# Kernel tuning notes

Measured on AMD Instinct MI355X. Metric: run time of the kernel, lower is better.

## Reference

```python
import jax, jax.numpy as jnp
import numpy as np

B, T, I = 32768, 28, 28
H, C = 128, 10


def setup_inputs() -> dict:
    key = jax.random.key(0)
    ks = jax.random.split(key, 7)
    s_u = 1.0 / np.sqrt(I)
    s_w = 1.0 / np.sqrt(H)
    return {
        "x": jax.random.normal(ks[0], (B, T, I), dtype=jnp.float32),
        "U_w": jax.random.uniform(ks[1], (H, I), jnp.float32, -s_u, s_u),
        "U_b": jax.random.uniform(ks[2], (H,), jnp.float32, -s_u, s_u),
        "W_w": jax.random.uniform(ks[3], (H, H), jnp.float32, -s_w, s_w),
        "W_b": jax.random.uniform(ks[4], (H,), jnp.float32, -s_w, s_w),
        "V_w": jax.random.uniform(ks[5], (C, H), jnp.float32, -s_w, s_w),
        "V_b": jax.random.uniform(ks[6], (C,), jnp.float32, -s_w, s_w),
    }


def reference(x, U_w, U_b, W_w, W_b, V_w, V_b):
    # x: [B, T, I]. Precompute input projections for all timesteps at once
    # (one big GEMM), then scan the sequential recurrence on S.
    ux = jnp.einsum("bti,hi->tbh", x, U_w) + U_b  # [T, B, H]

    def step(S, ux_t):
        S = jnp.tanh(ux_t + S @ W_w.T + W_b)
        return S, None

    S0 = jnp.zeros((x.shape[0], W_w.shape[0]), dtype=x.dtype)
    S_final, _ = jax.lax.scan(step, S0, ux)
    return S_final @ V_w.T + V_b  # [B, C]
```

## Files before the change

kernel.cpp:

```cpp
#include <hip/hip_runtime.h>


#define T_STEPS 28
#define S_STRIDE 132

typedef __attribute__((ext_vector_type(4))) float f32x4;
typedef __attribute__((ext_vector_type(8))) short short8;

#define MFMA16 __builtin_amdgcn_mfma_f32_16x16x32_bf16

__device__ __forceinline__ unsigned pack2(float lo, float hi) {
#if __has_builtin(__builtin_amdgcn_cvt_pk_bf16_f32)
  auto p = __builtin_amdgcn_cvt_pk_bf16_f32(lo, hi);
  return __builtin_bit_cast(unsigned, p);
#else
  unsigned a = __builtin_bit_cast(unsigned, lo);
  a += 0x7FFFu + ((a >> 16) & 1u);
  unsigned b = __builtin_bit_cast(unsigned, hi);
  b += 0x7FFFu + ((b >> 16) & 1u);
  return (a >> 16) | (b & 0xFFFF0000u);
#endif
}

__device__ __forceinline__ short8 to_frag(f32x4 a, f32x4 b) {
  union { unsigned u[4]; short8 v; } r;
  r.u[0] = pack2(a[0], a[1]);
  r.u[1] = pack2(a[2], a[3]);
  r.u[2] = pack2(b[0], b[1]);
  r.u[3] = pack2(b[2], b[3]);
  return r.v;
}

__device__ __forceinline__ short8 load_frag64(const unsigned short* sp, int off) {
  union { uint2 d[2]; short8 v; } r;
  r.d[0] = *(const uint2*)(sp + off);
  r.d[1] = *(const uint2*)(sp + off + 4);
  return r.v;
}

__device__ __forceinline__ f32x4 tanh4(f32x4 z) {
  f32x4 x2 = z * z;
  f32x4 p = 945.0f + x2 * (105.0f + x2);
  f32x4 q = 945.0f + x2 * (420.0f + 15.0f * x2);
  f32x4 num = z * p;
  f32x4 r;
#pragma unroll
  for (int i = 0; i < 4; ++i) r[i] = __builtin_amdgcn_rcpf(q[i]);
  f32x4 t = num * r;
#pragma unroll
  for (int i = 0; i < 4; ++i) t[i] = __builtin_amdgcn_fmed3f(t[i], -1.0f, 1.0f);
  return t;
}

__global__ __launch_bounds__(256, 4) void rnn_fused(
    const float* __restrict__ x,  const float* __restrict__ Uw,
    const float* __restrict__ Ub, const float* __restrict__ Ww,
    const float* __restrict__ Wb, const float* __restrict__ Vw,
    const float* __restrict__ Vb, float* __restrict__ out) {
  __shared__ __align__(16) unsigned short Sbuf[2][16 * S_STRIDE];

  const int tid  = threadIdx.x;
  const int w    = tid >> 6;
  const int lane = tid & 63;
  const int l15  = lane & 15;
  const int q    = lane >> 4;
  const int mrow = w * 32;
  const int b0   = blockIdx.x * 16;

  const f32x4 zero4 = {0.f, 0.f, 0.f, 0.f};

  const float* xp = x + (size_t)(b0 + l15) * 784 + q * 8;
  f32x4 xa = *(const f32x4*)xp;
  f32x4 xb = zero4;
  if (q < 3) xb = *(const f32x4*)(xp + 4);

  short8 wfrag[2][4];
  short8 ufrag[2];
  f32x4  bias[2];
#pragma unroll
  for (int mt = 0; mt < 2; ++mt) {
    const int h = mrow + mt * 16 + l15;
    const float* wp = Ww + h * 128 + q * 8;
#pragma unroll
    for (int kt = 0; kt < 4; ++kt) {
      wfrag[mt][kt] = to_frag(*(const f32x4*)wp, *(const f32x4*)(wp + 4));
      wp += 32;
    }
    const float* up = Uw + h * 28 + q * 8;
    f32x4 u0 = *(const f32x4*)up;
    f32x4 u1 = zero4;
    if (q < 3) u1 = *(const f32x4*)(up + 4);
    ufrag[mt] = to_frag(u0, u1);
    const int hb = mrow + mt * 16 + q * 4;
    bias[mt] = *(const f32x4*)(Wb + hb) + *(const f32x4*)(Ub + hb);
  }

  const int ro = l15 * S_STRIDE;

  {
    short8 xf = to_frag(xa, xb);
    const float* x1 = xp + 28;
    xa = *(const f32x4*)x1;
    if (q < 3) xb = *(const f32x4*)(x1 + 4);
    unsigned short* wp = &Sbuf[1][0];
#pragma unroll
    for (int mt = 0; mt < 2; ++mt) {
      f32x4 d0 = MFMA16(ufrag[mt], xf, bias[mt], 0, 0, 0);
      f32x4 t0 = tanh4(d0);
      uint2 dd; dd.x = pack2(t0[0], t0[1]); dd.y = pack2(t0[2], t0[3]);
      *(uint2*)(wp + ro + mrow + mt * 16 + q * 4) = dd;
    }
  }
  __syncthreads();

  const float* xn = xp + 56;
  f32x4 acc[2];
#pragma unroll 1
  for (int t = 1; t < T_STEPS; ++t) {
    short8 xf = to_frag(xa, xb);
    if (t < T_STEPS - 1) {
      xa = *(const f32x4*)xn;
      if (q < 3) xb = *(const f32x4*)(xn + 4);
      xn += 28;
    }

    const unsigned short* sp = &Sbuf[t & 1][0] + ro + q * 8;

    short8 sA = load_frag64(sp, 0);
#pragma unroll
    for (int mt = 0; mt < 2; ++mt)
      acc[mt] = MFMA16(wfrag[mt][0], sA, bias[mt], 0, 0, 0);
#pragma unroll
    for (int kt = 1; kt < 4; ++kt) {
      sA = load_frag64(sp, kt * 32);
#pragma unroll
      for (int mt = 0; mt < 2; ++mt)
        acc[mt] = MFMA16(wfrag[mt][kt], sA, acc[mt], 0, 0, 0);
    }
#pragma unroll
    for (int mt = 0; mt < 2; ++mt)
      acc[mt] = MFMA16(ufrag[mt], xf, acc[mt], 0, 0, 0);

    unsigned short* wp = &Sbuf[(t + 1) & 1][0];
#pragma unroll
    for (int mt = 0; mt < 2; ++mt) {
      f32x4 th = tanh4(acc[mt]);
      uint2 dd; dd.x = pack2(th[0], th[1]); dd.y = pack2(th[2], th[3]);
      *(uint2*)(wp + ro + mrow + mt * 16 + q * 4) = dd;
    }
    __syncthreads();
  }

  {
    const int r  = tid >> 4;
    const int c0 = tid & 15;
    if (c0 < 10) {
      const float* vp = Vw + c0 * 128;
      const unsigned short* srow = &Sbuf[0][0] + r * S_STRIDE;
      float a0 = Vb[c0];
#pragma unroll
      for (int h = 0; h < 128; h += 4) {
        uint2 d  = *(const uint2*)(srow + h);
        f32x4 v4 = *(const f32x4*)(vp + h);
        a0 += __builtin_bit_cast(float, d.x << 16) * v4[0];
        a0 += __builtin_bit_cast(float, d.x & 0xFFFF0000u) * v4[1];
        a0 += __builtin_bit_cast(float, d.y << 16) * v4[2];
        a0 += __builtin_bit_cast(float, d.y & 0xFFFF0000u) * v4[3];
      }
      out[(size_t)(b0 + r) * 10 + c0] = a0;
    }
  }
}

extern "C" void kernel_launch(void* const* d_in, const int* in_sizes, int n_in,
                              void* d_out, int out_size, void* d_ws, size_t ws_size,
                              hipStream_t stream) {
  const float* x  = (const float*)d_in[0];
  const float* Uw = (const float*)d_in[1];
  const float* Ub = (const float*)d_in[2];
  const float* Ww = (const float*)d_in[3];
  const float* Wb = (const float*)d_in[4];
  const float* Vw = (const float*)d_in[5];
  const float* Vb = (const float*)d_in[6];
  rnn_fused<<<2048, 256, 0, stream>>>(x, Uw, Ub, Ww, Wb, Vw, Vb, (float*)d_out);
}
```

Measured before the change: 216.0 us.

## Stage x timesteps into LDS in cooperative bf16 chunks

Replaces the per-timestep global loads of x, each wave loading its own fragment, with block-cooperative staging of 10-timestep chunks into a shared bf16 buffer. The block's 16 rows are read as contiguous float4 slots and converted once, and each step then reads its input fragment from LDS. The aim is better-coalesced global reads and less redundant conversion and load latency on the serial recurrence. The cost is extra LDS, which may reduce occupancy, plus two extra syncs where each chunk's global loads now sit on the critical path instead of being prefetched a step ahead.

Result: no change. 218.8 us (+1.3%).

```diff
diff --git a/kernel.cpp b/kernel.cpp
--- a/kernel.cpp
+++ b/kernel.cpp
@@ -3,6 +3,7 @@
 
 #define T_STEPS 28
 #define S_STRIDE 132
+#define X_STRIDE 324
 
 typedef __attribute__((ext_vector_type(4))) float f32x4;
 typedef __attribute__((ext_vector_type(8))) short short8;
@@ -52,12 +53,45 @@
   return t;
 }
 
+template <int NT>
+__device__ __forceinline__ void stage_chunk(const float* __restrict__ xblk,
+                                            unsigned short* __restrict__ Xb,
+                                            int tid, int t0) {
+  constexpr int SLOTS = 16 * NT * 7;
+  constexpr int ITERS = (SLOTS + 255) / 256;
+  f32x4 xr[ITERS];
+#pragma unroll
+  for (int k = 0; k < ITERS; ++k) {
+    const int s = tid + 256 * k;
+    if (s < SLOTS) {
+      const int row = s / (NT * 7), g = s - row * (NT * 7);
+      const int tt = g / 7, j = g - tt * 7;
+      xr[k] = *(const f32x4*)(xblk + row * 784 + (t0 + tt) * 28 + j * 4);
+    }
+  }
+#pragma unroll
+  for (int k = 0; k < ITERS; ++k) {
+    const int s = tid + 256 * k;
+    if (s < SLOTS) {
+      const int row = s / (NT * 7), g = s - row * (NT * 7);
+      const int tt = g / 7, j = g - tt * 7;
+      uint2 d; d.x = pack2(xr[k][0], xr[k][1]); d.y = pack2(xr[k][2], xr[k][3]);
+      *(uint2*)(Xb + row * X_STRIDE + tt * 32 + j * 4) = d;
+      if (j == 0) {
+        uint2 zz; zz.x = 0u; zz.y = 0u;
+        *(uint2*)(Xb + row * X_STRIDE + tt * 32 + 28) = zz;
+      }
+    }
+  }
+}
+
 __global__ __launch_bounds__(256, 4) void rnn_fused(
     const float* __restrict__ x,  const float* __restrict__ Uw,
     const float* __restrict__ Ub, const float* __restrict__ Ww,
     const float* __restrict__ Wb, const float* __restrict__ Vw,
     const float* __restrict__ Vb, float* __restrict__ out) {
   __shared__ __align__(16) unsigned short Sbuf[2][16 * S_STRIDE];
+  __shared__ __align__(16) unsigned short Xbuf[16 * X_STRIDE];
 
   const int tid  = threadIdx.x;
   const int w    = tid >> 6;
@@ -68,11 +102,9 @@
   const int b0   = blockIdx.x * 16;
 
   const f32x4 zero4 = {0.f, 0.f, 0.f, 0.f};
-
-  const float* xp = x + (size_t)(b0 + l15) * 784 + q * 8;
-  f32x4 xa = *(const f32x4*)xp;
-  f32x4 xb = zero4;
-  if (q < 3) xb = *(const f32x4*)(xp + 4);
+  const float* xblk = x + (size_t)b0 * 784;
+
+  stage_chunk<10>(xblk, Xbuf, tid, 0);
 
   short8 wfrag[2][4];
   short8 ufrag[2];
@@ -94,14 +126,43 @@
     const int hb = mrow + mt * 16 + q * 4;
     bias[mt] = *(const f32x4*)(Wb + hb) + *(const f32x4*)(Ub + hb);
   }
+  __syncthreads();
 
   const int ro = l15 * S_STRIDE;
+  const int xo = l15 * X_STRIDE + q * 8;
+  f32x4 acc[2];
+
+  auto step = [&](int t, int tt) {
+    short8 xf = load_frag64(&Xbuf[0], xo + tt * 32);
+    const unsigned short* sp = &Sbuf[t & 1][0] + ro + q * 8;
+
+    short8 sA = load_frag64(sp, 0);
+#pragma unroll
+    for (int mt = 0; mt < 2; ++mt)
+      acc[mt] = MFMA16(wfrag[mt][0], sA, bias[mt], 0, 0, 0);
+#pragma unroll
+    for (int kt = 1; kt < 4; ++kt) {
+      sA = load_frag64(sp, kt * 32);
+#pragma unroll
+      for (int mt = 0; mt < 2; ++mt)
+        acc[mt] = MFMA16(wfrag[mt][kt], sA, acc[mt], 0, 0, 0);
+    }
+#pragma unroll
+    for (int mt = 0; mt < 2; ++mt)
+      acc[mt] = MFMA16(ufrag[mt], xf, acc[mt], 0, 0, 0);
+
+    unsigned short* wp = &Sbuf[(t + 1) & 1][0];
+#pragma unroll
+    for (int mt = 0; mt < 2; ++mt) {
+      f32x4 th = tanh4(acc[mt]);
+      uint2 dd; dd.x = pack2(th[0], th[1]); dd.y = pack2(th[2], th[3]);
+      *(uint2*)(wp + ro + mrow + mt * 16 + q * 4) = dd;
+    }
+    __syncthreads();
+  };
 
   {
-    short8 xf = to_frag(xa, xb);
-    const float* x1 = xp + 28;
-    xa = *(const f32x4*)x1;
-    if (q < 3) xb = *(const f32x4*)(x1 + 4);
+    short8 xf = load_frag64(&Xbuf[0], xo);
     unsigned short* wp = &Sbuf[1][0];
 #pragma unroll
     for (int mt = 0; mt < 2; ++mt) {
@@ -113,43 +174,18 @@
   }
   __syncthreads();
 
-  const float* xn = xp + 56;
-  f32x4 acc[2];
 #pragma unroll 1
-  for (int t = 1; t < T_STEPS; ++t) {
-    short8 xf = to_frag(xa, xb);
-    if (t < T_STEPS - 1) {
-      xa = *(const f32x4*)xn;
-      if (q < 3) xb = *(const f32x4*)(xn + 4);
-      xn += 28;
-    }
-
-    const unsigned short* sp = &Sbuf[t & 1][0] + ro + q * 8;
-
-    short8 sA = load_frag64(sp, 0);
-#pragma unroll
-    for (int mt = 0; mt < 2; ++mt)
-      acc[mt] = MFMA16(wfrag[mt][0], sA, bias[mt], 0, 0, 0);
-#pragma unroll
-    for (int kt = 1; kt < 4; ++kt) {
-      sA = load_frag64(sp, kt * 32);
-#pragma unroll
-      for (int mt = 0; mt < 2; ++mt)
-        acc[mt] = MFMA16(wfrag[mt][kt], sA, acc[mt], 0, 0, 0);
-    }
-#pragma unroll
-    for (int mt = 0; mt < 2; ++mt)
-      acc[mt] = MFMA16(ufrag[mt], xf, acc[mt], 0, 0, 0);
-
-    unsigned short* wp = &Sbuf[(t + 1) & 1][0];
-#pragma unroll
-    for (int mt = 0; mt < 2; ++mt) {
-      f32x4 th = tanh4(acc[mt]);
-      uint2 dd; dd.x = pack2(th[0], th[1]); dd.y = pack2(th[2], th[3]);
-      *(uint2*)(wp + ro + mrow + mt * 16 + q * 4) = dd;
-    }
-    __syncthreads();
-  }
+  for (int t = 1; t < 10; ++t) step(t, t);
+
+  stage_chunk<10>(xblk, Xbuf, tid, 10);
+  __syncthreads();
+#pragma unroll 1
+  for (int t = 10; t < 20; ++t) step(t, t - 10);
+
+  stage_chunk<8>(xblk, Xbuf, tid, 20);
+  __syncthreads();
+#pragma unroll 1
+  for (int t = 20; t < T_STEPS; ++t) step(t, t - 20);
 
   {
     const int r  = tid >> 4;
```

## Process 32 batch rows per block with two independent MFMA chains

Applied to the files above, without the earlier changes.

Each block now handles 32 batch rows instead of 16, so the grid halves to 1024 blocks. Every wave reuses its register-resident W and U fragments across two independent 16-column batch tiles, which gives the MFMA pipeline two interleaved dependency chains per step and spreads each barrier over twice the work. The __syncthreads is replaced with an explicit lgkmcnt wait plus s_barrier. In exchange, accumulator and x registers roughly double and fewer blocks are resident, which may reduce occupancy.

Result: slower. 223.8 us (+3.6%).

```diff
diff --git a/kernel.cpp b/kernel.cpp
--- a/kernel.cpp
+++ b/kernel.cpp
@@ -52,12 +52,18 @@
   return t;
 }
 
+__device__ __forceinline__ void lds_barrier() {
+  asm volatile("s_waitcnt lgkmcnt(0)" ::: "memory");
+  __builtin_amdgcn_s_barrier();
+  asm volatile("" ::: "memory");
+}
+
 __global__ __launch_bounds__(256, 4) void rnn_fused(
     const float* __restrict__ x,  const float* __restrict__ Uw,
     const float* __restrict__ Ub, const float* __restrict__ Ww,
     const float* __restrict__ Wb, const float* __restrict__ Vw,
     const float* __restrict__ Vb, float* __restrict__ out) {
-  __shared__ __align__(16) unsigned short Sbuf[2][16 * S_STRIDE];
+  __shared__ __align__(16) unsigned short Sbuf[2][32 * S_STRIDE];
 
   const int tid  = threadIdx.x;
   const int w    = tid >> 6;
@@ -65,14 +71,15 @@
   const int l15  = lane & 15;
   const int q    = lane >> 4;
   const int mrow = w * 32;
-  const int b0   = blockIdx.x * 16;
+  const int b0   = blockIdx.x * 32;
 
   const f32x4 zero4 = {0.f, 0.f, 0.f, 0.f};
 
-  const float* xp = x + (size_t)(b0 + l15) * 784 + q * 8;
-  f32x4 xa = *(const f32x4*)xp;
-  f32x4 xb = zero4;
-  if (q < 3) xb = *(const f32x4*)(xp + 4);
+  const float* xp0 = x + (size_t)(b0 + l15) * 784 + q * 8;
+  const float* xp1 = xp0 + 16 * 784;
+  f32x4 xa0 = *(const f32x4*)xp0, xa1 = *(const f32x4*)xp1;
+  f32x4 xb0 = zero4, xb1 = zero4;
+  if (q < 3) { xb0 = *(const f32x4*)(xp0 + 4); xb1 = *(const f32x4*)(xp1 + 4); }
 
   short8 wfrag[2][4];
   short8 ufrag[2];
@@ -95,79 +102,100 @@
     bias[mt] = *(const f32x4*)(Wb + hb) + *(const f32x4*)(Ub + hb);
   }
 
-  const int ro = l15 * S_STRIDE;
+  const int ro0 = l15 * S_STRIDE;
+  const int ro1 = (16 + l15) * S_STRIDE;
+  const int dcol = mrow + q * 4;
 
   {
-    short8 xf = to_frag(xa, xb);
-    const float* x1 = xp + 28;
-    xa = *(const f32x4*)x1;
-    if (q < 3) xb = *(const f32x4*)(x1 + 4);
+    short8 xf0 = to_frag(xa0, xb0);
+    short8 xf1 = to_frag(xa1, xb1);
+    xa0 = *(const f32x4*)(xp0 + 28); xa1 = *(const f32x4*)(xp1 + 28);
+    if (q < 3) { xb0 = *(const f32x4*)(xp0 + 32); xb1 = *(const f32x4*)(xp1 + 32); }
     unsigned short* wp = &Sbuf[1][0];
 #pragma unroll
     for (int mt = 0; mt < 2; ++mt) {
-      f32x4 d0 = MFMA16(ufrag[mt], xf, bias[mt], 0, 0, 0);
+      f32x4 d0 = MFMA16(ufrag[mt], xf0, bias[mt], 0, 0, 0);
+      f32x4 d1 = MFMA16(ufrag[mt], xf1, bias[mt], 0, 0, 0);
       f32x4 t0 = tanh4(d0);
-      uint2 dd; dd.x = pack2(t0[0], t0[1]); dd.y = pack2(t0[2], t0[3]);
-      *(uint2*)(wp + ro + mrow + mt * 16 + q * 4) = dd;
-    }
-  }
-  __syncthreads();
-
-  const float* xn = xp + 56;
-  f32x4 acc[2];
+      f32x4 t1 = tanh4(d1);
+      uint2 e0; e0.x = pack2(t0[0], t0[1]); e0.y = pack2(t0[2], t0[3]);
+      uint2 e1; e1.x = pack2(t1[0], t1[1]); e1.y = pack2(t1[2], t1[3]);
+      *(uint2*)(wp + ro0 + dcol + mt * 16) = e0;
+      *(uint2*)(wp + ro1 + dcol + mt * 16) = e1;
+    }
+  }
+  lds_barrier();
+
+  f32x4 acc[2][2];
 #pragma unroll 1
   for (int t = 1; t < T_STEPS; ++t) {
-    short8 xf = to_frag(xa, xb);
+    short8 xf0 = to_frag(xa0, xb0);
+    short8 xf1 = to_frag(xa1, xb1);
     if (t < T_STEPS - 1) {
-      xa = *(const f32x4*)xn;
-      if (q < 3) xb = *(const f32x4*)(xn + 4);
-      xn += 28;
-    }
-
-    const unsigned short* sp = &Sbuf[t & 1][0] + ro + q * 8;
-
-    short8 sA = load_frag64(sp, 0);
-#pragma unroll
-    for (int mt = 0; mt < 2; ++mt)
-      acc[mt] = MFMA16(wfrag[mt][0], sA, bias[mt], 0, 0, 0);
+      const float* n0 = xp0 + (t + 1) * 28;
+      const float* n1 = xp1 + (t + 1) * 28;
+      xa0 = *(const f32x4*)n0; xa1 = *(const f32x4*)n1;
+      if (q < 3) { xb0 = *(const f32x4*)(n0 + 4); xb1 = *(const f32x4*)(n1 + 4); }
+    }
+
+    const unsigned short* sb = &Sbuf[t & 1][0] + q * 8;
+
+    short8 s0 = load_frag64(sb, ro0);
+    short8 s1 = load_frag64(sb, ro1);
+#pragma unroll
+    for (int mt = 0; mt < 2; ++mt) {
+      acc[mt][0] = MFMA16(wfrag[mt][0], s0, bias[mt], 0, 0, 0);
+      acc[mt][1] = MFMA16(wfrag[mt][0], s1, bias[mt], 0, 0, 0);
+    }
 #pragma unroll
     for (int kt = 1; kt < 4; ++kt) {
-      sA = load_frag64(sp, kt * 32);
-#pragma unroll
-      for (int mt = 0; mt < 2; ++mt)
-        acc[mt] = MFMA16(wfrag[mt][kt], sA, acc[mt], 0, 0, 0);
-    }
-#pragma unroll
-    for (int mt = 0; mt < 2; ++mt)
-      acc[mt] = MFMA16(ufrag[mt], xf, acc[mt], 0, 0, 0);
+      s0 = load_frag64(sb, ro0 + kt * 32);
+      s1 = load_frag64(sb, ro1 + kt * 32);
+#pragma unroll
+      for (int mt = 0; mt < 2; ++mt) {
+        acc[mt][0] = MFMA16(wfrag[mt][kt], s0, acc[mt][0], 0, 0, 0);
+        acc[mt][1] = MFMA16(wfrag[mt][kt], s1, acc[mt][1], 0, 0, 0);
+      }
+    }
+#pragma unroll
+    for (int mt = 0; mt < 2; ++mt) {
+      acc[mt][0] = MFMA16(ufrag[mt], xf0, acc[mt][0], 0, 0, 0);
+      acc[mt][1] = MFMA16(ufrag[mt], xf1, acc[mt][1], 0, 0, 0);
+    }
 
     unsigned short* wp = &Sbuf[(t + 1) & 1][0];
 #pragma unroll
     for (int mt = 0; mt < 2; ++mt) {
-      f32x4 th = tanh4(acc[mt]);
-      uint2 dd; dd.x = pack2(th[0], th[1]); dd.y = pack2(th[2], th[3]);
-      *(uint2*)(wp + ro + mrow + mt * 16 + q * 4) = dd;
-    }
-    __syncthreads();
+      f32x4 t0 = tanh4(acc[mt][0]);
+      f32x4 t1 = tanh4(acc[mt][1]);
+      uint2 e0; e0.x = pack2(t0[0], t0[1]); e0.y = pack2(t0[2], t0[3]);
+      uint2 e1; e1.x = pack2(t1[0], t1[1]); e1.y = pack2(t1[2], t1[3]);
+      *(uint2*)(wp + ro0 + dcol + mt * 16) = e0;
+      *(uint2*)(wp + ro1 + dcol + mt * 16) = e1;
+    }
+    lds_barrier();
   }
 
   {
-    const int r  = tid >> 4;
     const int c0 = tid & 15;
     if (c0 < 10) {
       const float* vp = Vw + c0 * 128;
-      const unsigned short* srow = &Sbuf[0][0] + r * S_STRIDE;
-      float a0 = Vb[c0];
-#pragma unroll
-      for (int h = 0; h < 128; h += 4) {
-        uint2 d  = *(const uint2*)(srow + h);
-        f32x4 v4 = *(const f32x4*)(vp + h);
-        a0 += __builtin_bit_cast(float, d.x << 16) * v4[0];
-        a0 += __builtin_bit_cast(float, d.x & 0xFFFF0000u) * v4[1];
-        a0 += __builtin_bit_cast(float, d.y << 16) * v4[2];
-        a0 += __builtin_bit_cast(float, d.y & 0xFFFF0000u) * v4[3];
+#pragma unroll
+      for (int half = 0; half < 2; ++half) {
+        const int r = half * 16 + (tid >> 4);
+        const unsigned short* srow = &Sbuf[0][0] + r * S_STRIDE;
+        float a0 = Vb[c0];
+#pragma unroll
+        for (int h = 0; h < 128; h += 4) {
+          uint2 d  = *(const uint2*)(srow + h);
+          f32x4 v4 = *(const f32x4*)(vp + h);
+          a0 += __builtin_bit_cast(float, d.x << 16) * v4[0];
+          a0 += __builtin_bit_cast(float, d.x & 0xFFFF0000u) * v4[1];
+          a0 += __builtin_bit_cast(float, d.y << 16) * v4[2];
+          a0 += __builtin_bit_cast(float, d.y & 0xFFFF0000u) * v4[3];
+        }
+        out[(size_t)(b0 + r) * 10 + c0] = a0;
       }
-      out[(size_t)(b0 + r) * 10 + c0] = a0;
     }
   }
 }
@@ -182,5 +210,5 @@
   const float* Wb = (const float*)d_in[4];
   const float* Vw = (const float*)d_in[5];
   const float* Vb = (const float*)d_in[6];
-  rnn_fused<<<2048, 256, 0, stream>>>(x, Uw, Ub, Ww, Wb, Vw, Vb, (float*)d_out);
-}
+  rnn_fused<<<1024, 256, 0, stream>>>(x, Uw, Ub, Ww, Wb, Vw, Vb, (float*)d_out);
+}
```
